# Performance work log

Measured on AMD Instinct MI355X. Metric: run time of the kernel, lower is better.

The kernel has to match this reference:

```python
import jax, jax.numpy as jnp
import numpy as np

N_LAYERS = 2
DIN = 128
DOUT = 128


def _uniform(key, shape, std):
    return jax.random.uniform(key, shape, jnp.float32, -std, std)


def setup_inputs() -> dict:
    key = jax.random.key(0)
    ks = jax.random.split(key, 12)
    B, T, N, F = 2, 8, 10000, DIN
    E = 320000
    x = jax.random.normal(ks[0], (B, T, N, F), jnp.float32)
    edge_index = jax.random.randint(ks[1], (2, E), 0, N, jnp.int64)
    edge_weight = jax.random.uniform(ks[2], (E,), jnp.float32)
    std_w = 1.0 / np.sqrt(DOUT)
    std_p = 1.0 / np.sqrt(DIN)
    std_g = 1.0 / np.sqrt(DIN)  # torch GRUCell init: U(-1/sqrt(H), 1/sqrt(H))
    W0 = _uniform(ks[3], (N_LAYERS, DIN, DOUT), std_w)
    p = _uniform(ks[4], (N_LAYERS, DIN, 1), std_p)
    w_ih = _uniform(ks[5], (N_LAYERS, 3 * DIN, DIN), std_g)
    w_hh = _uniform(ks[6], (N_LAYERS, 3 * DIN, DIN), std_g)
    b_ih = _uniform(ks[7], (N_LAYERS, 3 * DIN), std_g)
    b_hh = _uniform(ks[8], (N_LAYERS, 3 * DIN), std_g)
    bias = jnp.zeros((N_LAYERS, DOUT), jnp.float32)
    return {"x": x, "edge_index": edge_index, "edge_weight": edge_weight,
            "W0": W0, "p": p, "w_ih": w_ih, "w_hh": w_hh,
            "b_ih": b_ih, "b_hh": b_hh, "bias": bias}


def _gru_cell(xg, hg, wih, whh, bih, bhh):
    # torch.nn.GRUCell: gate order r, z, n
    gi = xg @ wih.T + bih
    gh = hg @ whh.T + bhh
    ir, iz, inn = jnp.split(gi, 3, axis=-1)
    hr, hz, hn = jnp.split(gh, 3, axis=-1)
    r = jax.nn.sigmoid(ir + hr)
    z = jax.nn.sigmoid(iz + hz)
    n = jnp.tanh(inn + r * hn)
    return (1.0 - z) * n + z * hg


def _topk_pool(xb, pc, k):
    # xb: [b, N, din], pc: [din, 1] -> [b, k, din]
    scores = (xb @ pc)[..., 0] / jnp.linalg.norm(pc)  # [b, N]
    vals, idx = jax.lax.top_k(scores, k)               # [b, k], sorted desc
    g = jnp.take_along_axis(xb, idx[..., None], axis=1)  # [b, k, din]
    return g * jnp.tanh(vals)[..., None]


def reference(x, edge_index, edge_weight, W0, p, w_ih, w_hh, b_ih, b_hh, bias):
    B, T, N, F = x.shape
    dout = W0.shape[-1]
    # --- GCN symmetric normalization with self-loops (done once, static graph) ---
    src, tgt = edge_index[0], edge_index[1]
    loops = jnp.arange(N, dtype=src.dtype)
    row = jnp.concatenate([src, loops])
    col = jnp.concatenate([tgt, loops])
    w = jnp.concatenate([edge_weight, jnp.ones((N,), x.dtype)])
    deg = jnp.zeros((N,), x.dtype).at[col].add(w)
    dinv = jnp.where(deg > 0, deg ** -0.5, 0.0)
    wn = dinv[row] * w * dinv[col]  # [E+N]

    def step(Ws, xt):
        out = xt  # [b, N, din]
        new_Ws = []
        for c in range(N_LAYERS):
            W = Ws[c]  # [b, din, dout]
            din = W.shape[1]
            pooled = _topk_pool(out, p[c], dout)                 # [b, dout, din]
            hg = W.transpose(0, 2, 1).reshape(B * dout, din)     # (b dout) din
            xg = pooled.reshape(B * dout, din)
            hg = _gru_cell(xg, hg, w_ih[c], w_hh[c], b_ih[c], b_hh[c])
            W = hg.reshape(B, dout, din).transpose(0, 2, 1)      # [b, din, dout]
            o = jnp.einsum('bnd,bde->bne', out, W)               # [b, N, dout]
            # gather-scale-scatter propagation (aggr='add')
            m = o[:, row, :] * wn[None, :, None]                 # [b, E+N, dout]
            o = jnp.zeros((B, N, dout), x.dtype).at[:, col, :].add(m)
            o = o + bias[c]
            out = jax.nn.relu(o)
            new_Ws.append(W)
        return tuple(new_Ws), out

    Ws0 = tuple(jnp.broadcast_to(W0[c], (B,) + W0[c].shape) for c in range(N_LAYERS))
    _, outs = jax.lax.scan(step, Ws0, jnp.moveaxis(x, 1, 0))
    return outs[-1]  # output at final step, [b, N, hidden]
```

## Files before the change

### kernel.cpp

```cpp
#include <hip/hip_runtime.h>
#include <hip/hip_bf16.h>
#include <math.h>


#define BB 2
#define TT 8
#define FF 128
#define GG 384
#define BINS 8192
#define CAP 512

typedef float v4f __attribute__((ext_vector_type(4)));

__device__ __forceinline__ float bf2f(unsigned short u) {
  return __uint_as_float((unsigned)u << 16);
}
__device__ __forceinline__ unsigned short f2bf(float f) {
  unsigned x = __float_as_uint(f);
  unsigned r = ((x >> 16) & 1u) + 0x7fffu;
  return (unsigned short)((x + r) >> 16);
}

__global__ void prep_kernel(const int* __restrict__ ei32, int E, int* __restrict__ flag,
                            const float* __restrict__ p, float* __restrict__ pinv) {
  if (blockIdx.x == 0) {
    int step = E / 256;
    int e = threadIdx.x * step;
    if (ei32[2 * e + 1] != 0) *flag = 1;
  } else {
    int c = blockIdx.x - 1, tid = threadIdx.x;
    float s = 0.f;
    if (tid < 128) { float v = p[c * FF + tid]; s = v * v; }
    for (int o = 32; o; o >>= 1) s += __shfl_xor(s, o, 64);
    __shared__ float red[4];
    if ((tid & 63) == 0) red[tid >> 6] = s;
    __syncthreads();
    if (tid == 0) pinv[c] = 1.0f / sqrtf(red[0] + red[1] + red[2] + red[3]);
  }
}

__device__ __forceinline__ void edge_fetch(const void* ei, int is32, int E,
                                           int e, const float* ew,
                                           int& row, int& col, float& w) {
  if (e < E) {
    if (is32) {
      const int* p = (const int*)ei;
      row = p[e]; col = p[E + e];
    } else {
      const long long* p = (const long long*)ei;
      row = (int)p[e]; col = (int)p[(long long)E + e];
    }
    w = ew[e];
  } else {
    row = col = e - E; w = 1.0f;
  }
}

__global__ void hist_kernel(const void* ei, const int* flag, int E, int N,
                            const float* __restrict__ ew,
                            float* __restrict__ deg, int* __restrict__ counts) {
  int e = blockIdx.x * 256 + threadIdx.x;
  if (e >= E + N) return;
  int row, col; float w;
  edge_fetch(ei, *flag, E, e, ew, row, col, w);
  atomicAdd(&deg[col], w);
  atomicAdd(&counts[col], 1);
}

__global__ __launch_bounds__(1024) void scan_kernel(
    const int* __restrict__ counts, const float* __restrict__ deg,
    int* __restrict__ offsets, float* __restrict__ dinv, int N, int EN) {
  __shared__ int wtot[16];
  int tid = threadIdx.x, lane = tid & 63, wid = tid >> 6;
  int base = tid * 10;
  int lc[10]; int s10 = 0;
#pragma unroll
  for (int q = 0; q < 10; ++q) {
    int idx = base + q;
    int cv = (idx < N) ? counts[idx] : 0;
    lc[q] = cv; s10 += cv;
    if (idx < N) {
      float d = deg[idx];
      dinv[idx] = (d > 0.f) ? 1.0f / sqrtf(d) : 0.f;
    }
  }
  int s = s10;
#pragma unroll
  for (int off = 1; off <= 32; off <<= 1) {
    int v = __shfl_up(s, off, 64);
    if (lane >= off) s += v;
  }
  if (lane == 63) wtot[wid] = s;
  __syncthreads();
  int pre = 0;
  for (int w2 = 0; w2 < wid; ++w2) pre += wtot[w2];
  int run = pre + s - s10;
#pragma unroll
  for (int q = 0; q < 10; ++q) {
    int idx = base + q;
    if (idx < N) { offsets[idx] = run; run += lc[q]; }
  }
  if (tid == 0) offsets[N] = EN;
}

__global__ void scatter_kernel(const void* ei, const int* flag, int E, int N,
                               const float* __restrict__ ew,
                               const float* __restrict__ dinv,
                               const int* __restrict__ offs,
                               int* __restrict__ cursors,
                               int2* __restrict__ ep) {
  int e = blockIdx.x * 256 + threadIdx.x;
  if (e >= E + N) return;
  int row, col; float w;
  edge_fetch(ei, *flag, E, e, ew, row, col, w);
  int pos = atomicAdd(&cursors[col], 1);
  ep[offs[col] + pos] = make_int2(row, __float_as_int(dinv[row] * w * dinv[col]));
}

template <int SRC_BF16>
__global__ __launch_bounds__(256) void prop_kernel(
    const void* __restrict__ srcv, size_t s_tstride, size_t s_bstride,
    float* __restrict__ dst, size_t d_tstride, size_t d_bstride,
    const int2* __restrict__ ep, const int* __restrict__ offs,
    const float* __restrict__ p, const float* __restrict__ pinv,
    unsigned long long* __restrict__ keys, int* __restrict__ hist,
    int N, int NG, int t8) {
  constexpr int PER = SRC_BF16 ? 8 : 4;
  constexpr int RSU = SRC_BF16 ? 16 : 32;
  int lid = blockIdx.x;
  int t, s;
  if (t8) { t = lid & 7; s = lid >> 3; } else { t = 0; s = lid; }
  int fq = s / NG, vg = s - fq * NG;
  int lane = threadIdx.x & 63;
  int e = lane >> 3, sub = lane & 7;
  int v = vg * 4 + (threadIdx.x >> 6);
  if (v >= N) return;
  int e0 = offs[v], e1 = offs[v + 1];
  size_t o0 = (size_t)t * s_tstride, o1 = o0 + s_bstride;
  const uint4* g0;
  const uint4* g1;
  if constexpr (SRC_BF16) {
    g0 = (const uint4*)((const unsigned short*)srcv + o0);
    g1 = (const uint4*)((const unsigned short*)srcv + o1);
  } else {
    g0 = (const uint4*)((const float*)srcv + o0);
    g1 = (const uint4*)((const float*)srcv + o1);
  }
  int fqs = fq * 8;
  float acc0[PER], acc1[PER];
#pragma unroll
  for (int q = 0; q < PER; ++q) { acc0[q] = 0.f; acc1[q] = 0.f; }
  for (int base = e0; base < e1; base += 64) {
    int cnt = e1 - base; if (cnt > 64) cnt = 64;
    int2 m = make_int2(0, 0);
    if (lane < cnt) m = ep[base + lane];
    for (int i = 0; i < cnt; i += 8) {
      int srcl = i + e;
      int row = __shfl(m.x, srcl, 64);
      float wv = __int_as_float(__shfl(m.y, srcl, 64));
      if (srcl >= cnt) wv = 0.f;
      size_t r = (size_t)row * RSU + fqs + sub;
      uint4 ra = g0[r], rb = g1[r];
      if constexpr (SRC_BF16) {
        acc0[0] += wv * bf2f(ra.x & 0xffff); acc0[1] += wv * bf2f(ra.x >> 16);
        acc0[2] += wv * bf2f(ra.y & 0xffff); acc0[3] += wv * bf2f(ra.y >> 16);
        acc0[4] += wv * bf2f(ra.z & 0xffff); acc0[5] += wv * bf2f(ra.z >> 16);
        acc0[6] += wv * bf2f(ra.w & 0xffff); acc0[7] += wv * bf2f(ra.w >> 16);
        acc1[0] += wv * bf2f(rb.x & 0xffff); acc1[1] += wv * bf2f(rb.x >> 16);
        acc1[2] += wv * bf2f(rb.y & 0xffff); acc1[3] += wv * bf2f(rb.y >> 16);
        acc1[4] += wv * bf2f(rb.z & 0xffff); acc1[5] += wv * bf2f(rb.z >> 16);
        acc1[6] += wv * bf2f(rb.w & 0xffff); acc1[7] += wv * bf2f(rb.w >> 16);
      } else {
        acc0[0] += wv * __uint_as_float(ra.x);
        acc0[1] += wv * __uint_as_float(ra.y);
        acc0[2] += wv * __uint_as_float(ra.z);
        acc0[3] += wv * __uint_as_float(ra.w);
        acc1[0] += wv * __uint_as_float(rb.x);
        acc1[1] += wv * __uint_as_float(rb.y);
        acc1[2] += wv * __uint_as_float(rb.z);
        acc1[3] += wv * __uint_as_float(rb.w);
      }
    }
  }
#pragma unroll
  for (int mk = 8; mk <= 32; mk <<= 1) {
#pragma unroll
    for (int q = 0; q < PER; ++q) {
      acc0[q] += __shfl_xor(acc0[q], mk, 64);
      acc1[q] += __shfl_xor(acc1[q], mk, 64);
    }
  }
  if (e < 2) {
    float* ob = dst + (size_t)t * d_tstride + (e ? d_bstride : 0);
    float* av = e ? acc1 : acc0;
    size_t fo = (size_t)v * FF + fq * (PER * 8) + sub * PER;
    v4f st0 = {av[0], av[1], av[2], av[3]};
    __builtin_nontemporal_store(st0, (v4f*)(ob + fo));
    if constexpr (SRC_BF16) {
      v4f st1 = {av[4], av[5], av[6], av[7]};
      __builtin_nontemporal_store(st1, (v4f*)(ob + fo + 4));
    }
  }
  if constexpr (!SRC_BF16) {
    if (p && fq == 0) {
      int half = lane >> 5, i32 = lane & 31;
      const v4f* xrow = (const v4f*)(half ? g1 : g0);
      v4f xv = __builtin_nontemporal_load(xrow + (size_t)v * 32 + i32);
      float4 pp = ((const float4*)p)[i32];
      float sc = xv.x * pp.x + xv.y * pp.y + xv.z * pp.z + xv.w * pp.w;
#pragma unroll
      for (int o = 1; o <= 16; o <<= 1) sc += __shfl_xor(sc, o, 64);
      if (i32 == 0) {
        float ss = sc * (*pinv);
        unsigned u = __float_as_uint(ss);
        u = (u & 0x80000000u) ? ~u : (u | 0x80000000u);
        int tb = t * 2 + half;
        keys[(size_t)tb * N + v] = ((unsigned long long)u << 32) | (unsigned)(~v);
        atomicAdd(&hist[tb * BINS + (u >> 19)], 1);
      }
    }
  }
}

__device__ __forceinline__ unsigned long long shfl_xor_u64(unsigned long long x,
                                                           int m) {
  unsigned lo = (unsigned)x, hi = (unsigned)(x >> 32);
  lo = __shfl_xor(lo, m, 64);
  hi = __shfl_xor(hi, m, 64);
  return ((unsigned long long)hi << 32) | lo;
}

__global__ __launch_bounds__(1024) void selectsort_kernel(
    const unsigned long long* __restrict__ keys, const int* __restrict__ hist,
    int N, int* __restrict__ idx_sel, float* __restrict__ gate_sel) {
  int tb = blockIdx.y * 2 + blockIdx.x, tid = threadIdx.x;
  int lane = tid & 63, wid = tid >> 6;
  const int* h = hist + tb * BINS;
  __shared__ int wtot[16];
  __shared__ unsigned long long cand[CAP];
  __shared__ int sT, ncnt;
  int base = tid * 8;
  int lc[8]; int local = 0;
#pragma unroll
  for (int q = 0; q < 8; ++q) { lc[q] = h[base + q]; local += lc[q]; }
  if (tid == 0) ncnt = 0;
  int s = local;
#pragma unroll
  for (int off = 1; off <= 32; off <<= 1) {
    int v = __shfl_down(s, off, 64);
    if (lane + off < 64) s += v;
  }
  if (lane == 0) wtot[wid] = s;
  __syncthreads();
  int above_w = 0;
  for (int w2 = wid + 1; w2 < 16; ++w2) above_w += wtot[w2];
  int incl = above_w + s;
  int above = incl - local;
  if (above < 128 && incl >= 128) {
    int cnt = above;
#pragma unroll
    for (int q = 7; q >= 0; --q) {
      int c = lc[q];
      if (cnt + c >= 128) { sT = base + q; break; }
      cnt += c;
    }
  }
  __syncthreads();
  int T = sT;
  for (int i = tid; i < N; i += 1024) {
    unsigned long long kk = keys[(size_t)tb * N + i];
    if ((int)(kk >> 51) >= T) {
      int pos = atomicAdd(&ncnt, 1);
      if (pos < CAP) cand[pos] = kk;
    }
  }
  __syncthreads();
  if (tid < 64) {
    int nc = ncnt < CAP ? ncnt : CAP;
    unsigned long long v[8];
#pragma unroll
    for (int r = 0; r < 8; ++r) {
      int e = r * 64 + lane;
      v[r] = (e < nc) ? cand[e] : 0ULL;
    }
    for (int k = 2; k <= 512; k <<= 1)
      for (int j = k >> 1; j > 0; j >>= 1) {
        if (j >= 64) {
          int rj = j >> 6;
#pragma unroll
          for (int r = 0; r < 8; ++r)
            if (!(r & rj)) {
              int r2 = r | rj;
              bool up = (((r * 64) & k) != 0);
              unsigned long long a = v[r], c = v[r2];
              bool sw = up ? (a > c) : (a < c);
              if (sw) { v[r] = c; v[r2] = a; }
            }
        } else {
#pragma unroll
          for (int r = 0; r < 8; ++r) {
            unsigned long long o = shfl_xor_u64(v[r], j);
            int e = r * 64 + lane;
            bool up = (e & k) != 0;
            bool lower = (lane & j) == 0;
            unsigned long long mn = v[r] < o ? v[r] : o;
            unsigned long long mx = v[r] < o ? o : v[r];
            v[r] = (lower == up) ? mn : mx;
          }
        }
      }
#pragma unroll
    for (int r = 0; r < 2; ++r) {
      int e = r * 64 + lane;
      unsigned long long kk = v[r];
      unsigned n = ~((unsigned)kk);
      unsigned u = (unsigned)(kk >> 32);
      float sc = (u & 0x80000000u) ? __uint_as_float(u & 0x7FFFFFFFu)
                                   : __uint_as_float(~u);
      idx_sel[tb * 128 + e] = (int)n;
      gate_sel[tb * 128 + e] = tanhf(sc);
    }
  }
}

template <int SRC_BF16>
__global__ __launch_bounds__(256) void wchain_kernel(
    const void* __restrict__ srcv, size_t src_tstride, size_t src_bstride,
    const int* __restrict__ idx_sel, const float* __restrict__ gate_sel,
    const float* __restrict__ Winit,
    const float* __restrict__ wih, const float* __restrict__ whh,
    const float* __restrict__ bih, const float* __restrict__ bhh,
    float* __restrict__ snap) {
  int b = blockIdx.x, j0 = blockIdx.y * 4;
  int tid = threadIdx.x, side = tid >> 7, kl = tid & 127;
  __shared__ float pooled[4][FF];
  __shared__ float hbuf[4][FF];
  __shared__ float ghbuf[3][4][FF];
  for (int e = tid; e < 4 * FF; e += 256) {
    int j = e >> 7, m = e & 127;
    hbuf[j][m] = Winit[m * FF + j0 + j];
  }
  float b0 = side ? bhh[kl] : bih[kl];
  float b1 = side ? bhh[FF + kl] : bih[FF + kl];
  float b2 = side ? bhh[2 * FF + kl] : bih[2 * FF + kl];
  const float* wmat = side ? whh : wih;
  const float4* w0p = (const float4*)(wmat + (size_t)(0 * FF + kl) * FF);
  const float4* w1p = (const float4*)(wmat + (size_t)(1 * FF + kl) * FF);
  const float4* w2p = (const float4*)(wmat + (size_t)(2 * FF + kl) * FF);
  for (int t = 0; t < TT; ++t) {
    int tb = t * 2 + b;
    __syncthreads();
    for (int e = tid; e < 4 * FF; e += 256) {
      int j = e >> 7, m = e & 127;
      int n = idx_sel[tb * 128 + j0 + j];
      float g = gate_sel[tb * 128 + j0 + j];
      size_t off = (size_t)t * src_tstride + (size_t)b * src_bstride +
                   (size_t)n * FF + m;
      float xv;
      if constexpr (SRC_BF16) xv = bf2f(((const unsigned short*)srcv)[off]);
      else                    xv = ((const float*)srcv)[off];
      pooled[j][m] = xv * g;
    }
    __syncthreads();
    const float4* vsrc = (const float4*)(side ? &hbuf[0][0] : &pooled[0][0]);
    float acc0[4] = {}, acc1[4] = {}, acc2[4] = {};
    for (int mq = 0; mq < 32; ++mq) {
      float4 w0 = w0p[mq], w1 = w1p[mq], w2 = w2p[mq];
#pragma unroll
      for (int j = 0; j < 4; ++j) {
        float4 v = vsrc[j * 32 + mq];
        acc0[j] += v.x * w0.x + v.y * w0.y + v.z * w0.z + v.w * w0.w;
        acc1[j] += v.x * w1.x + v.y * w1.y + v.z * w1.z + v.w * w1.w;
        acc2[j] += v.x * w2.x + v.y * w2.y + v.z * w2.z + v.w * w2.w;
      }
    }
    if (side) {
#pragma unroll
      for (int j = 0; j < 4; ++j) {
        ghbuf[0][j][kl] = acc0[j] + b0;
        ghbuf[1][j][kl] = acc1[j] + b1;
        ghbuf[2][j][kl] = acc2[j] + b2;
      }
    }
    __syncthreads();
    if (!side) {
#pragma unroll
      for (int j = 0; j < 4; ++j) {
        float rr = 1.0f / (1.0f + expf(-(acc0[j] + b0 + ghbuf[0][j][kl])));
        float zz = 1.0f / (1.0f + expf(-(acc1[j] + b1 + ghbuf[1][j][kl])));
        float nn = tanhf(acc2[j] + b2 + rr * ghbuf[2][j][kl]);
        float h = hbuf[j][kl];
        float hn = (1.0f - zz) * nn + zz * h;
        hbuf[j][kl] = hn;
        snap[((size_t)tb * FF + kl) * FF + j0 + j] = hn;
      }
    }
  }
}

__global__ __launch_bounds__(256) void gemm_kernel(
    const float* __restrict__ A, size_t a_tstride, size_t a_bstride,
    const float* __restrict__ Wsnap, const float* __restrict__ bias,
    float* __restrict__ outf, unsigned short* __restrict__ outb,
    size_t o_tstride, size_t o_bstride,
    const float* __restrict__ p1, const float* __restrict__ pinv1,
    unsigned long long* __restrict__ keys, int* __restrict__ hist, int N) {
  int nb = blockIdx.x, b = blockIdx.y, t = blockIdx.z;
  int tb = t * 2 + b;
  __shared__ float Ast[32][132];
  __shared__ float Bs[32][128];
  __shared__ float spart[128][17];
  __shared__ float p1s[128];
  int tid = threadIdx.x;
  int tc = tid & 15, tr = tid >> 4;
  if (p1 && tid < 128) p1s[tid] = p1[tid];
  float acc[8][8] = {};
  const float* Ab = A + (size_t)t * a_tstride + (size_t)b * a_bstride;
  const float* Wb = Wsnap + (size_t)tb * FF * FF;
  for (int kc = 0; kc < 4; ++kc) {
    int k0 = kc * 32;
    __syncthreads();
    for (int e = tid; e < 128 * 32; e += 256) {
      int r = e >> 5, kk = e & 31;
      int n = nb * 128 + r;
      Ast[kk][r] = (n < N) ? Ab[(size_t)n * FF + k0 + kk] : 0.f;
    }
    for (int e = tid; e < 32 * 128; e += 256) {
      int r = e >> 7, dd = e & 127;
      Bs[r][dd] = Wb[(k0 + r) * FF + dd];
    }
    __syncthreads();
#pragma unroll 4
    for (int kk = 0; kk < 32; ++kk) {
      const float4* arow = (const float4*)Ast[kk];
      float4 a0 = arow[tr * 2], a1 = arow[tr * 2 + 1];
      const float4* brow = (const float4*)Bs[kk];
      float4 b0 = brow[tc * 2], b1 = brow[tc * 2 + 1];
      float av[8] = {a0.x, a0.y, a0.z, a0.w, a1.x, a1.y, a1.z, a1.w};
      float bv[8] = {b0.x, b0.y, b0.z, b0.w, b1.x, b1.y, b1.z, b1.w};
#pragma unroll
      for (int i = 0; i < 8; ++i)
#pragma unroll
        for (int j = 0; j < 8; ++j) acc[i][j] += av[i] * bv[j];
    }
  }
  float bb[8];
#pragma unroll
  for (int j = 0; j < 8; ++j) bb[j] = bias[tc * 8 + j];
  size_t obase = (size_t)t * o_tstride + (size_t)b * o_bstride;
#pragma unroll
  for (int i = 0; i < 8; ++i) {
    int n = nb * 128 + tr * 8 + i;
    float v[8]; float part = 0.f;
#pragma unroll
    for (int j = 0; j < 8; ++j) {
      v[j] = fmaxf(acc[i][j] + bb[j], 0.f);
      if (p1) part += v[j] * p1s[tc * 8 + j];
    }
    if (n < N) {
      if (outb) {
        unsigned short* dst = outb + obase + (size_t)n * FF + tc * 8;
        uint4 pk;
        pk.x = (unsigned)f2bf(v[0]) | ((unsigned)f2bf(v[1]) << 16);
        pk.y = (unsigned)f2bf(v[2]) | ((unsigned)f2bf(v[3]) << 16);
        pk.z = (unsigned)f2bf(v[4]) | ((unsigned)f2bf(v[5]) << 16);
        pk.w = (unsigned)f2bf(v[6]) | ((unsigned)f2bf(v[7]) << 16);
        *(uint4*)dst = pk;
      } else {
        float4* dst = (float4*)(outf + obase + (size_t)n * FF + tc * 8);
        dst[0] = make_float4(v[0], v[1], v[2], v[3]);
        dst[1] = make_float4(v[4], v[5], v[6], v[7]);
      }
    }
    if (p1) spart[tr * 8 + i][tc] = part;
  }
  if (p1) {
    __syncthreads();
    if (tid < 128) {
      int n = nb * 128 + tid;
      if (n < N) {
        float s = 0.f;
#pragma unroll
        for (int q = 0; q < 16; ++q) s += spart[tid][q];
        s *= *pinv1;
        unsigned u = __float_as_uint(s);
        u = (u & 0x80000000u) ? ~u : (u | 0x80000000u);
        keys[(size_t)tb * N + n] = ((unsigned long long)u << 32) | (unsigned)(~n);
        atomicAdd(&hist[tb * BINS + (u >> 19)], 1);
      }
    }
  }
}

extern "C" void kernel_launch(void* const* d_in, const int* in_sizes, int n_in,
                              void* d_out, int out_size, void* d_ws, size_t ws_size,
                              hipStream_t stream) {
  const float* x   = (const float*)d_in[0];
  const void*  ei  = d_in[1];
  const float* ew  = (const float*)d_in[2];
  const float* W0  = (const float*)d_in[3];
  const float* p   = (const float*)d_in[4];
  const float* wih = (const float*)d_in[5];
  const float* whh = (const float*)d_in[6];
  const float* bih = (const float*)d_in[7];
  const float* bhh = (const float*)d_in[8];
  const float* bias= (const float*)d_in[9];

  const int E  = in_sizes[2];
  const int N  = in_sizes[0] / (BB * TT * FF);
  const int EN = E + N;
  const size_t NF = (size_t)N * FF;
  const int NG = (N + 3) / 4;

  char* w = (char*)d_ws;
  auto alloc = [&](size_t bytes) -> char* {
    char* r = w; w += (bytes + 255) & ~(size_t)255; return r;
  };
  char* zbeg = w;
  float* deg      = (float*)alloc((size_t)N * 4);
  int*   counts   = (int*)  alloc((size_t)N * 4);
  int*   cursors  = (int*)  alloc((size_t)N * 4);
  int*   flag     = (int*)  alloc(4);
  int*   hist     = (int*)  alloc((size_t)2 * TT * BB * BINS * 4);
  char* zend = w;
  int*   offsets  = (int*)  alloc((size_t)(N + 1) * 4);
  float* dinv     = (float*)alloc((size_t)N * 4);
  float* pinv     = (float*)alloc(2 * 4);
  int2*  ep       = (int2*) alloc((size_t)EN * 8);
  unsigned long long* keys0 = (unsigned long long*)alloc((size_t)TT * BB * N * 8);
  unsigned long long* keys1 = (unsigned long long*)alloc((size_t)TT * BB * N * 8);
  int*   idx0     = (int*)  alloc((size_t)TT * BB * 128 * 4);
  float* gate0    = (float*)alloc((size_t)TT * BB * 128 * 4);
  int*   idx1     = (int*)  alloc((size_t)TT * BB * 128 * 4);
  float* gate1    = (float*)alloc((size_t)TT * BB * 128 * 4);
  float* W0snap   = (float*)alloc((size_t)TT * BB * FF * FF * 4);
  float* W1snap   = (float*)alloc((size_t)TT * BB * FF * FF * 4);
  float* xp       = (float*)alloc((size_t)TT * BB * NF * 4);
  unsigned short* act0 = (unsigned short*)alloc((size_t)TT * BB * NF * 2);
  float* xq       = (float*)alloc((size_t)BB * NF * 4);
  int* hist0 = hist;
  int* hist1 = hist + (size_t)TT * BB * BINS;

  hipMemsetAsync(zbeg, 0, (size_t)(zend - zbeg), stream);

  prep_kernel<<<3, 256, 0, stream>>>((const int*)ei, E, flag, p, pinv);
  hist_kernel<<<(EN + 255) / 256, 256, 0, stream>>>(ei, flag, E, N, ew, deg, counts);
  scan_kernel<<<1, 1024, 0, stream>>>(counts, deg, offsets, dinv, N, EN);
  scatter_kernel<<<(EN + 255) / 256, 256, 0, stream>>>(ei, flag, E, N, ew, dinv,
                                                       offsets, cursors, ep);

  prop_kernel<0><<<NG * 4 * TT, 256, 0, stream>>>(
      x, NF, (size_t)TT * NF, xp, (size_t)BB * NF, NF,
      ep, offsets, p, pinv, keys0, hist0, N, NG, 1);

  selectsort_kernel<<<dim3(BB, TT), 1024, 0, stream>>>(
      keys0, hist0, N, idx0, gate0);

  wchain_kernel<0><<<dim3(BB, 32), 256, 0, stream>>>(
      x, NF, (size_t)TT * NF, idx0, gate0, W0,
      wih, whh, bih, bhh, W0snap);

  gemm_kernel<<<dim3((N + 127) / 128, BB, TT), 256, 0, stream>>>(
      xp, (size_t)BB * NF, NF, W0snap, bias,
      nullptr, act0, (size_t)BB * NF, NF,
      p + FF, pinv + 1, keys1, hist1, N);

  selectsort_kernel<<<dim3(BB, TT), 1024, 0, stream>>>(
      keys1, hist1, N, idx1, gate1);

  wchain_kernel<1><<<dim3(BB, 32), 256, 0, stream>>>(
      act0, (size_t)BB * NF, NF, idx1, gate1, W0 + FF * FF,
      wih + (size_t)GG * FF, whh + (size_t)GG * FF,
      bih + GG, bhh + GG, W1snap);

  prop_kernel<1><<<NG * 2, 256, 0, stream>>>(
      act0 + (size_t)(TT - 1) * BB * NF, 0, NF, xq, 0, NF,
      ep, offsets, nullptr, nullptr, nullptr, nullptr, N, NG, 0);

  gemm_kernel<<<dim3((N + 127) / 128, BB, 1), 256, 0, stream>>>(
      xq, 0, NF, W1snap + (size_t)(TT - 1) * BB * FF * FF, bias + FF,
      (float*)d_out, nullptr, 0, NF,
      nullptr, nullptr, nullptr, nullptr, N);
}
```

Baseline: 837.4 us.

## Process two timesteps per block in fp32 propagation and change GEMM A-tile layout

The fp32 propagation kernel is restructured so each block handles two timesteps and both batches for a 16-float feature slice. It gathers four rows per edge and reduces across lanes with a butterfly exchange, which amortizes edge-list loads and shuffles over more work. The bf16 path is split into its own kernel. The GEMM's shared A tile changes from a transposed layout to row-major with padding, so the transpose store is removed but inner-loop reads become scalar instead of float4. Both changes risk register pressure and extra shared-memory read instructions.

```diff
diff --git a/kernel.cpp b/kernel.cpp
--- a/kernel.cpp
+++ b/kernel.cpp
@@ -117,39 +117,129 @@
   ep[offs[col] + pos] = make_int2(row, __float_as_int(dinv[row] * w * dinv[col]));
 }
 
-template <int SRC_BF16>
-__global__ __launch_bounds__(256) void prop_kernel(
-    const void* __restrict__ srcv, size_t s_tstride, size_t s_bstride,
+__global__ __launch_bounds__(256) void prop2_kernel(
+    const float* __restrict__ x, size_t s_tstride, size_t s_bstride,
     float* __restrict__ dst, size_t d_tstride, size_t d_bstride,
     const int2* __restrict__ ep, const int* __restrict__ offs,
     const float* __restrict__ p, const float* __restrict__ pinv,
     unsigned long long* __restrict__ keys, int* __restrict__ hist,
-    int N, int NG, int t8) {
-  constexpr int PER = SRC_BF16 ? 8 : 4;
-  constexpr int RSU = SRC_BF16 ? 16 : 32;
+    int N, int NG) {
   int lid = blockIdx.x;
-  int t, s;
-  if (t8) { t = lid & 7; s = lid >> 3; } else { t = 0; s = lid; }
-  int fq = s / NG, vg = s - fq * NG;
+  int tp = lid & 3;
+  int fq0 = (lid >> 2) & 1;
+  int s = lid >> 3;
+  int fqh = s / NG, vg = s - fqh * NG;
+  int fq = fqh * 2 + fq0;
+  int lane = threadIdx.x & 63;
+  int e = lane >> 2, sub = lane & 3;
+  int v = vg * 4 + (threadIdx.x >> 6);
+  if (v >= N) return;
+  int e0 = offs[v], e1 = offs[v + 1];
+  int t0 = tp * 2;
+  const uint4* g00 = (const uint4*)(x + (size_t)t0 * s_tstride);
+  const uint4* g01 = (const uint4*)(x + (size_t)t0 * s_tstride + s_bstride);
+  const uint4* g10 = (const uint4*)(x + (size_t)(t0 + 1) * s_tstride);
+  const uint4* g11 = (const uint4*)(x + (size_t)(t0 + 1) * s_tstride + s_bstride);
+  int fo16 = fq * 4 + sub;
+  float a00[4] = {}, a01[4] = {}, a10[4] = {}, a11[4] = {};
+  for (int base = e0; base < e1; base += 64) {
+    int cnt = e1 - base; if (cnt > 64) cnt = 64;
+    int2 m = make_int2(0, 0);
+    if (lane < cnt) m = ep[base + lane];
+    for (int i = 0; i < cnt; i += 16) {
+      int srcl = i + e;
+      int row = __shfl(m.x, srcl, 64);
+      float wv = __int_as_float(__shfl(m.y, srcl, 64));
+      if (srcl >= cnt) wv = 0.f;
+      size_t r = (size_t)row * 32 + fo16;
+      uint4 r00 = g00[r], r01 = g01[r], r10 = g10[r], r11 = g11[r];
+      a00[0] += wv * __uint_as_float(r00.x);
+      a00[1] += wv * __uint_as_float(r00.y);
+      a00[2] += wv * __uint_as_float(r00.z);
+      a00[3] += wv * __uint_as_float(r00.w);
+      a01[0] += wv * __uint_as_float(r01.x);
+      a01[1] += wv * __uint_as_float(r01.y);
+      a01[2] += wv * __uint_as_float(r01.z);
+      a01[3] += wv * __uint_as_float(r01.w);
+      a10[0] += wv * __uint_as_float(r10.x);
+      a10[1] += wv * __uint_as_float(r10.y);
+      a10[2] += wv * __uint_as_float(r10.z);
+      a10[3] += wv * __uint_as_float(r10.w);
+      a11[0] += wv * __uint_as_float(r11.x);
+      a11[1] += wv * __uint_as_float(r11.y);
+      a11[2] += wv * __uint_as_float(r11.z);
+      a11[3] += wv * __uint_as_float(r11.w);
+    }
+  }
+  bool hi5 = (lane & 32) != 0;
+  float k0[4], k1[4];
+#pragma unroll
+  for (int q = 0; q < 4; ++q) {
+    float s0 = hi5 ? a10[q] : a00[q];
+    float s1 = hi5 ? a11[q] : a01[q];
+    float o0 = hi5 ? a00[q] : a10[q];
+    float o1 = hi5 ? a01[q] : a11[q];
+    k0[q] = s0 + __shfl_xor(o0, 32, 64);
+    k1[q] = s1 + __shfl_xor(o1, 32, 64);
+  }
+  bool hi4 = (lane & 16) != 0;
+  float kk[4];
+#pragma unroll
+  for (int q = 0; q < 4; ++q) {
+    float sK = hi4 ? k1[q] : k0[q];
+    float oK = hi4 ? k0[q] : k1[q];
+    kk[q] = sK + __shfl_xor(oK, 16, 64);
+  }
+#pragma unroll
+  for (int q = 0; q < 4; ++q) {
+    kk[q] += __shfl_xor(kk[q], 8, 64);
+    kk[q] += __shfl_xor(kk[q], 4, 64);
+  }
+  if ((e & 3) == 0) {
+    int tt = e >> 3, b = (e >> 2) & 1;
+    float* ob = dst + (size_t)(t0 + tt) * d_tstride + (b ? d_bstride : 0);
+    size_t fo = (size_t)v * FF + fq * 16 + sub * 4;
+    v4f st = {kk[0], kk[1], kk[2], kk[3]};
+    __builtin_nontemporal_store(st, (v4f*)(ob + fo));
+  }
+  if (p && fq == 0) {
+    int half = lane >> 5, i32 = lane & 31;
+    float4 pp = ((const float4*)p)[i32];
+#pragma unroll
+    for (int tt = 0; tt < 2; ++tt) {
+      const v4f* xr = (const v4f*)(half ? (tt ? g11 : g01) : (tt ? g10 : g00));
+      v4f xv = __builtin_nontemporal_load(xr + (size_t)v * 32 + i32);
+      float sc = xv.x * pp.x + xv.y * pp.y + xv.z * pp.z + xv.w * pp.w;
+#pragma unroll
+      for (int o = 1; o <= 16; o <<= 1) sc += __shfl_xor(sc, o, 64);
+      if (i32 == 0) {
+        float ss = sc * (*pinv);
+        unsigned u = __float_as_uint(ss);
+        u = (u & 0x80000000u) ? ~u : (u | 0x80000000u);
+        int tb = (t0 + tt) * 2 + half;
+        keys[(size_t)tb * N + v] = ((unsigned long long)u << 32) | (unsigned)(~v);
+        atomicAdd(&hist[tb * BINS + (u >> 19)], 1);
+      }
+    }
+  }
+}
+
+__global__ __launch_bounds__(256) void propb_kernel(
+    const unsigned short* __restrict__ srcv, size_t s_bstride,
+    float* __restrict__ dst, size_t d_bstride,
+    const int2* __restrict__ ep, const int* __restrict__ offs,
+    int N, int NG) {
+  int lid = blockIdx.x;
+  int fq = lid / NG, vg = lid - fq * NG;
   int lane = threadIdx.x & 63;
   int e = lane >> 3, sub = lane & 7;
   int v = vg * 4 + (threadIdx.x >> 6);
   if (v >= N) return;
   int e0 = offs[v], e1 = offs[v + 1];
-  size_t o0 = (size_t)t * s_tstride, o1 = o0 + s_bstride;
-  const uint4* g0;
-  const uint4* g1;
-  if constexpr (SRC_BF16) {
-    g0 = (const uint4*)((const unsigned short*)srcv + o0);
-    g1 = (const uint4*)((const unsigned short*)srcv + o1);
-  } else {
-    g0 = (const uint4*)((const float*)srcv + o0);
-    g1 = (const uint4*)((const float*)srcv + o1);
-  }
+  const uint4* g0 = (const uint4*)srcv;
+  const uint4* g1 = (const uint4*)(srcv + s_bstride);
   int fqs = fq * 8;
-  float acc0[PER], acc1[PER];
-#pragma unroll
-  for (int q = 0; q < PER; ++q) { acc0[q] = 0.f; acc1[q] = 0.f; }
+  float acc0[8] = {}, acc1[8] = {};
   for (int base = e0; base < e1; base += 64) {
     int cnt = e1 - base; if (cnt > 64) cnt = 64;
     int2 m = make_int2(0, 0);
@@ -159,66 +249,34 @@
       int row = __shfl(m.x, srcl, 64);
       float wv = __int_as_float(__shfl(m.y, srcl, 64));
       if (srcl >= cnt) wv = 0.f;
-      size_t r = (size_t)row * RSU + fqs + sub;
+      size_t r = (size_t)row * 16 + fqs + sub;
       uint4 ra = g0[r], rb = g1[r];
-      if constexpr (SRC_BF16) {
-        acc0[0] += wv * bf2f(ra.x & 0xffff); acc0[1] += wv * bf2f(ra.x >> 16);
-        acc0[2] += wv * bf2f(ra.y & 0xffff); acc0[3] += wv * bf2f(ra.y >> 16);
-        acc0[4] += wv * bf2f(ra.z & 0xffff); acc0[5] += wv * bf2f(ra.z >> 16);
-        acc0[6] += wv * bf2f(ra.w & 0xffff); acc0[7] += wv * bf2f(ra.w >> 16);
-        acc1[0] += wv * bf2f(rb.x & 0xffff); acc1[1] += wv * bf2f(rb.x >> 16);
-        acc1[2] += wv * bf2f(rb.y & 0xffff); acc1[3] += wv * bf2f(rb.y >> 16);
-        acc1[4] += wv * bf2f(rb.z & 0xffff); acc1[5] += wv * bf2f(rb.z >> 16);
-        acc1[6] += wv * bf2f(rb.w & 0xffff); acc1[7] += wv * bf2f(rb.w >> 16);
-      } else {
-        acc0[0] += wv * __uint_as_float(ra.x);
-        acc0[1] += wv * __uint_as_float(ra.y);
-        acc0[2] += wv * __uint_as_float(ra.z);
-        acc0[3] += wv * __uint_as_float(ra.w);
-        acc1[0] += wv * __uint_as_float(rb.x);
-        acc1[1] += wv * __uint_as_float(rb.y);
-        acc1[2] += wv * __uint_as_float(rb.z);
-        acc1[3] += wv * __uint_as_float(rb.w);
-      }
+      acc0[0] += wv * bf2f(ra.x & 0xffff); acc0[1] += wv * bf2f(ra.x >> 16);
+      acc0[2] += wv * bf2f(ra.y & 0xffff); acc0[3] += wv * bf2f(ra.y >> 16);
+      acc0[4] += wv * bf2f(ra.z & 0xffff); acc0[5] += wv * bf2f(ra.z >> 16);
+      acc0[6] += wv * bf2f(ra.w & 0xffff); acc0[7] += wv * bf2f(ra.w >> 16);
+      acc1[0] += wv * bf2f(rb.x & 0xffff); acc1[1] += wv * bf2f(rb.x >> 16);
+      acc1[2] += wv * bf2f(rb.y & 0xffff); acc1[3] += wv * bf2f(rb.y >> 16);
+      acc1[4] += wv * bf2f(rb.z & 0xffff); acc1[5] += wv * bf2f(rb.z >> 16);
+      acc1[6] += wv * bf2f(rb.w & 0xffff); acc1[7] += wv * bf2f(rb.w >> 16);
     }
   }
 #pragma unroll
   for (int mk = 8; mk <= 32; mk <<= 1) {
 #pragma unroll
-    for (int q = 0; q < PER; ++q) {
+    for (int q = 0; q < 8; ++q) {
       acc0[q] += __shfl_xor(acc0[q], mk, 64);
       acc1[q] += __shfl_xor(acc1[q], mk, 64);
     }
   }
   if (e < 2) {
-    float* ob = dst + (size_t)t * d_tstride + (e ? d_bstride : 0);
+    float* ob = dst + (e ? d_bstride : 0);
     float* av = e ? acc1 : acc0;
-    size_t fo = (size_t)v * FF + fq * (PER * 8) + sub * PER;
+    size_t fo = (size_t)v * FF + fq * 64 + sub * 8;
     v4f st0 = {av[0], av[1], av[2], av[3]};
+    v4f st1 = {av[4], av[5], av[6], av[7]};
     __builtin_nontemporal_store(st0, (v4f*)(ob + fo));
-    if constexpr (SRC_BF16) {
-      v4f st1 = {av[4], av[5], av[6], av[7]};
-      __builtin_nontemporal_store(st1, (v4f*)(ob + fo + 4));
-    }
-  }
-  if constexpr (!SRC_BF16) {
-    if (p && fq == 0) {
-      int half = lane >> 5, i32 = lane & 31;
-      const v4f* xrow = (const v4f*)(half ? g1 : g0);
-      v4f xv = __builtin_nontemporal_load(xrow + (size_t)v * 32 + i32);
-      float4 pp = ((const float4*)p)[i32];
-      float sc = xv.x * pp.x + xv.y * pp.y + xv.z * pp.z + xv.w * pp.w;
-#pragma unroll
-      for (int o = 1; o <= 16; o <<= 1) sc += __shfl_xor(sc, o, 64);
-      if (i32 == 0) {
-        float ss = sc * (*pinv);
-        unsigned u = __float_as_uint(ss);
-        u = (u & 0x80000000u) ? ~u : (u | 0x80000000u);
-        int tb = t * 2 + half;
-        keys[(size_t)tb * N + v] = ((unsigned long long)u << 32) | (unsigned)(~v);
-        atomicAdd(&hist[tb * BINS + (u >> 19)], 1);
-      }
-    }
+    __builtin_nontemporal_store(st1, (v4f*)(ob + fo + 4));
   }
 }
 
@@ -407,7 +465,7 @@
     unsigned long long* __restrict__ keys, int* __restrict__ hist, int N) {
   int nb = blockIdx.x, b = blockIdx.y, t = blockIdx.z;
   int tb = t * 2 + b;
-  __shared__ float Ast[32][132];
+  __shared__ float As[128][33];
   __shared__ float Bs[32][128];
   __shared__ float spart[128][17];
   __shared__ float p1s[128];
@@ -423,7 +481,7 @@
     for (int e = tid; e < 128 * 32; e += 256) {
       int r = e >> 5, kk = e & 31;
       int n = nb * 128 + r;
-      Ast[kk][r] = (n < N) ? Ab[(size_t)n * FF + k0 + kk] : 0.f;
+      As[r][kk] = (n < N) ? Ab[(size_t)n * FF + k0 + kk] : 0.f;
     }
     for (int e = tid; e < 32 * 128; e += 256) {
       int r = e >> 7, dd = e & 127;
@@ -432,11 +490,11 @@
     __syncthreads();
 #pragma unroll 4
     for (int kk = 0; kk < 32; ++kk) {
-      const float4* arow = (const float4*)Ast[kk];
-      float4 a0 = arow[tr * 2], a1 = arow[tr * 2 + 1];
+      float av[8];
+#pragma unroll
+      for (int i = 0; i < 8; ++i) av[i] = As[tr * 8 + i][kk];
       const float4* brow = (const float4*)Bs[kk];
       float4 b0 = brow[tc * 2], b1 = brow[tc * 2 + 1];
-      float av[8] = {a0.x, a0.y, a0.z, a0.w, a1.x, a1.y, a1.z, a1.w};
       float bv[8] = {b0.x, b0.y, b0.z, b0.w, b1.x, b1.y, b1.z, b1.w};
 #pragma unroll
       for (int i = 0; i < 8; ++i)
@@ -549,9 +607,9 @@
   scatter_kernel<<<(EN + 255) / 256, 256, 0, stream>>>(ei, flag, E, N, ew, dinv,
                                                        offsets, cursors, ep);
 
-  prop_kernel<0><<<NG * 4 * TT, 256, 0, stream>>>(
+  prop2_kernel<<<NG * 32, 256, 0, stream>>>(
       x, NF, (size_t)TT * NF, xp, (size_t)BB * NF, NF,
-      ep, offsets, p, pinv, keys0, hist0, N, NG, 1);
+      ep, offsets, p, pinv, keys0, hist0, N, NG);
 
   selectsort_kernel<<<dim3(BB, TT), 1024, 0, stream>>>(
       keys0, hist0, N, idx0, gate0);
@@ -573,9 +631,9 @@
       wih + (size_t)GG * FF, whh + (size_t)GG * FF,
       bih + GG, bhh + GG, W1snap);
 
-  prop_kernel<1><<<NG * 2, 256, 0, stream>>>(
-      act0 + (size_t)(TT - 1) * BB * NF, 0, NF, xq, 0, NF,
-      ep, offsets, nullptr, nullptr, nullptr, nullptr, N, NG, 0);
+  propb_kernel<<<NG * 2, 256, 0, stream>>>(
+      act0 + (size_t)(TT - 1) * BB * NF, NF, xq, NF,
+      ep, offsets, N, NG);
 
   gemm_kernel<<<dim3((N + 127) / 128, BB, 1), 256, 0, stream>>>(
       xq, 0, NF, W1snap + (size_t)(TT - 1) * BB * FF * FF, bias + FF,
```

After: 948.6 us. 1.13x slower.
